# Kernel optimization log

Hardware: AMD Instinct MI355X
Metric: run time of the kernel (lower is better)

Reference implementation:

```python
import jax, jax.numpy as jnp
import numpy as np

D, H, L, V, BS = 1024, 16, 12, 50257, 2048
HD = D // H
EPS = 1e-5


def _ln(x, w, b):
    m = jnp.mean(x, -1, keepdims=True)
    v = jnp.mean(jnp.square(x - m), -1, keepdims=True)
    return (x - m) * jax.lax.rsqrt(v + EPS) * w + b


def setup_inputs() -> dict:
    key = jax.random.key(0)
    ks = jax.random.split(key, 10)
    B, T = 4, 1024
    s = 0.02
    return {
        "idx": jax.random.randint(ks[0], (B, T), 0, V),
        "targets": jax.random.randint(ks[1], (B, T), 0, V),
        "wte": s * jax.random.normal(ks[2], (V, D), jnp.float32),
        "wpe": s * jax.random.normal(ks[3], (BS, D), jnp.float32),
        "ln1_w": jnp.ones((L, D), jnp.float32),
        "ln1_b": jnp.zeros((L, D), jnp.float32),
        "qkv_w": s * jax.random.normal(ks[4], (L, D, 3 * D), jnp.float32),
        "qkv_b": jnp.zeros((L, 3 * D), jnp.float32),
        "o_w": s * jax.random.normal(ks[5], (L, D, D), jnp.float32),
        "o_b": jnp.zeros((L, D), jnp.float32),
        "ln2_w": jnp.ones((L, D), jnp.float32),
        "ln2_b": jnp.zeros((L, D), jnp.float32),
        "up_w": s * jax.random.normal(ks[6], (L, D, 4 * D), jnp.float32),
        "up_b": jnp.zeros((L, 4 * D), jnp.float32),
        "down_w": s * jax.random.normal(ks[7], (L, 4 * D, D), jnp.float32),
        "down_b": jnp.zeros((L, D), jnp.float32),
        "lnf_w": jnp.ones((D,), jnp.float32),
        "lnf_b": jnp.zeros((D,), jnp.float32),
        "lm_b": jnp.zeros((V,), jnp.float32),
    }


def _gpt(idx, targets, wte, wpe, ln1_w, ln1_b, qkv_w, qkv_b, o_w, o_b,
         ln2_w, ln2_b, up_w, up_b, down_w, down_b, lnf_w, lnf_b, lm_b):
    B, T = idx.shape
    x = wte[idx] + wpe[:T][None, :, :]  # [B,T,D]
    causal = jnp.tril(jnp.ones((T, T), bool))
    scale = HD ** -0.5

    def block(h, p):
        (l1w, l1b, qw, qb, ow, ob, l2w, l2b, uw, ub, dw, db) = p
        y = _ln(h, l1w, l1b)
        qkv = y @ qw + qb  # [B,T,3D]
        q, k, v = jnp.split(qkv, 3, axis=-1)
        q = q.reshape(B, T, H, HD)
        k = k.reshape(B, T, H, HD)
        v = v.reshape(B, T, H, HD)
        scores = jnp.einsum('bqhd,bkhd->bhqk', q, k) * scale
        scores = jnp.where(causal, scores, -jnp.inf)
        attn = jax.nn.softmax(scores, axis=-1)
        o = jnp.einsum('bhqk,bkhd->bqhd', attn, v).reshape(B, T, D)
        h = h + o @ ow + ob
        y = _ln(h, l2w, l2b)
        y = jax.nn.gelu(y @ uw + ub, approximate=False)
        h = h + y @ dw + db
        return h, None

    params = (ln1_w, ln1_b, qkv_w, qkv_b, o_w, o_b, ln2_w, ln2_b, up_w, up_b, down_w, down_b)
    x, _ = jax.lax.scan(block, x, params)
    x = _ln(x, lnf_w, lnf_b)
    logits = x @ wte.T + lm_b  # tied lm_head weight
    logp = jax.nn.log_softmax(logits, axis=-1)
    nll = -jnp.take_along_axis(logp, targets[..., None], axis=-1)[..., 0]
    loss = jnp.mean(nll)
    return logits, loss


def reference(idx, targets, wte, wpe, ln1_w, ln1_b, qkv_w, qkv_b, o_w, o_b,
              ln2_w, ln2_b, up_w, up_b, down_w, down_b, lnf_w, lnf_b, lm_b):
    return _gpt(idx, targets, wte, wpe, ln1_w, ln1_b, qkv_w, qkv_b, o_w, o_b,
                ln2_w, ln2_b, up_w, up_b, down_w, down_b, lnf_w, lnf_b, lm_b)
```

## Files before the change

### kernel.cpp

```cpp
#include <hip/hip_runtime.h>
#include <hip/hip_bf16.h>
#include <math.h>

typedef __attribute__((ext_vector_type(8))) short bfrag;
typedef __attribute__((ext_vector_type(4))) float f32x4;

static constexpr int Dm = 1024, Hh = 16, HD = 64, Ll = 12, Tt = 1024, Bb = 4;
static constexpr int Vv = 50257, Mrows = 4096;

__device__ inline unsigned short f2bf(float f) {
    unsigned u = __float_as_uint(f);
    u += 0x7fffu + ((u >> 16) & 1u);
    return (unsigned short)(u >> 16);
}
__device__ inline float bf2f(unsigned short s) {
    return __uint_as_float(((unsigned)s) << 16);
}

__device__ inline void gload16(const unsigned short* g, unsigned short* l) {
    __builtin_amdgcn_global_load_lds(
        (const __attribute__((address_space(1))) void*)g,
        (__attribute__((address_space(3))) void*)l, 16, 0, 0);
}

__global__ __launch_bounds__(256)
void embed_kernel(float* __restrict__ x, const float* __restrict__ wte,
                  const float* __restrict__ wpe, const int* __restrict__ idx) {
    int row = blockIdx.x;
    int t = row & (Tt - 1);
    int id = idx[row];
    int c = threadIdx.x * 4;
    float4 a = *reinterpret_cast<const float4*>(&wte[(size_t)id * Dm + c]);
    float4 p = *reinterpret_cast<const float4*>(&wpe[(size_t)t * Dm + c]);
    float4 o;
    o.x = a.x + p.x; o.y = a.y + p.y; o.z = a.z + p.z; o.w = a.w + p.w;
    *reinterpret_cast<float4*>(&x[(size_t)row * Dm + c]) = o;
}

__global__ __launch_bounds__(256)
void ln_kernel(unsigned short* __restrict__ y, const float* __restrict__ x,
               const float* __restrict__ w, const float* __restrict__ b) {
    int row = blockIdx.x;
    int tid = threadIdx.x;
    int lane = tid & 63, wv = tid >> 6;
    const float* xr = x + (size_t)row * Dm;
    float4 v = *reinterpret_cast<const float4*>(&xr[tid * 4]);
    float s1 = v.x + v.y + v.z + v.w;
    float s2 = v.x * v.x + v.y * v.y + v.z * v.z + v.w * v.w;
#pragma unroll
    for (int off = 1; off < 64; off <<= 1) {
        s1 += __shfl_xor(s1, off);
        s2 += __shfl_xor(s2, off);
    }
    __shared__ float r1[4], r2[4];
    if (lane == 0) { r1[wv] = s1; r2[wv] = s2; }
    __syncthreads();
    s1 = r1[0] + r1[1] + r1[2] + r1[3];
    s2 = r2[0] + r2[1] + r2[2] + r2[3];
    float mean = s1 * (1.0f / Dm);
    float var = s2 * (1.0f / Dm) - mean * mean;
    float rstd = rsqrtf(var + 1e-5f);
    float4 wvv = *reinterpret_cast<const float4*>(&w[tid * 4]);
    float4 bv = *reinterpret_cast<const float4*>(&b[tid * 4]);
    ushort4 o;
    o.x = f2bf((v.x - mean) * rstd * wvv.x + bv.x);
    o.y = f2bf((v.y - mean) * rstd * wvv.y + bv.y);
    o.z = f2bf((v.z - mean) * rstd * wvv.z + bv.z);
    o.w = f2bf((v.w - mean) * rstd * wvv.w + bv.w);
    *reinterpret_cast<ushort4*>(&y[(size_t)row * Dm + tid * 4]) = o;
}

__global__ __launch_bounds__(256)
void transpose_layer(const float* __restrict__ qw, const float* __restrict__ ow,
                     const float* __restrict__ uw, const float* __restrict__ dw,
                     unsigned short* __restrict__ wTq, unsigned short* __restrict__ wTo,
                     unsigned short* __restrict__ wTu, unsigned short* __restrict__ wTd) {
    __shared__ float t[32][33];
    int tb = blockIdx.x;
    const float* src; unsigned short* dst; int K, N, nx, base;
    if (tb < 3072)      { src = qw; dst = wTq; K = 1024; N = 3072; nx = 96;  base = 0; }
    else if (tb < 4096) { src = ow; dst = wTo; K = 1024; N = 1024; nx = 32;  base = 3072; }
    else if (tb < 8192) { src = uw; dst = wTu; K = 1024; N = 4096; nx = 128; base = 4096; }
    else                { src = dw; dst = wTd; K = 4096; N = 1024; nx = 32;  base = 8192; }
    int tt = tb - base;
    int n0 = (tt % nx) * 32, k0 = (tt / nx) * 32;
    int tid = threadIdx.x;
    int r = tid >> 3, c4 = (tid & 7) * 4;
    float4 v = *reinterpret_cast<const float4*>(&src[(size_t)(k0 + r) * N + n0 + c4]);
    t[r][c4] = v.x; t[r][c4 + 1] = v.y; t[r][c4 + 2] = v.z; t[r][c4 + 3] = v.w;
    __syncthreads();
    int nr = tid >> 3, kc = (tid & 7) * 4;
    ushort4 o;
    o.x = f2bf(t[kc][nr]);
    o.y = f2bf(t[kc + 1][nr]);
    o.z = f2bf(t[kc + 2][nr]);
    o.w = f2bf(t[kc + 3][nr]);
    *reinterpret_cast<ushort4*>(&dst[(size_t)(n0 + nr) * K + k0 + kc]) = o;
}

__global__ __launch_bounds__(128)
void cvt_rows(unsigned short* __restrict__ dst, const float* __restrict__ src) {
    int row = blockIdx.x;
    int t = threadIdx.x;
    const float* s = src + (size_t)row * Dm + t * 8;
    float4 f0 = *reinterpret_cast<const float4*>(s);
    float4 f1 = *reinterpret_cast<const float4*>(s + 4);
    ushort4 o0, o1;
    o0.x = f2bf(f0.x); o0.y = f2bf(f0.y); o0.z = f2bf(f0.z); o0.w = f2bf(f0.w);
    o1.x = f2bf(f1.x); o1.y = f2bf(f1.y); o1.z = f2bf(f1.z); o1.w = f2bf(f1.w);
    unsigned short* d = dst + (size_t)row * Dm + t * 8;
    *reinterpret_cast<ushort4*>(d) = o0;
    *reinterpret_cast<ushort4*>(d + 4) = o1;
}

template<int EPI, int GN>
__global__ __launch_bounds__(512, 1)
void gemm256(const unsigned short* __restrict__ A, const unsigned short* __restrict__ B,
             const float* __restrict__ bias, void* __restrict__ Cp,
             int Nv, int K, int ldc, int ncol) {
    __shared__ unsigned short As[4][256 * 32];
    __shared__ unsigned short Bs[4][256 * 32];
    const int tid = threadIdx.x;
    const int lane = tid & 63, w = tid >> 6;
    const int wr = w >> 2, wc = w & 3;
    const int g = lane >> 4, lr = lane & 15;
    const int slotk = (lr >> 1) & 3;

    const int gx = gridDim.x;
    int flat = blockIdx.y * gx + blockIdx.x;
    int nwg = gx * gridDim.y;
    {
        int q = nwg >> 3, rr = nwg & 7;
        int xcd = flat & 7, pos = flat >> 3;
        flat = ((xcd < rr) ? (xcd * (q + 1)) : (rr * (q + 1) + (xcd - rr) * q)) + pos;
    }
    const int bm = (flat % gx) * 256;
    const int bn = (flat / gx) * 256;

    const int srow = lane >> 2;
    const int gsrc = (lane & 3) ^ ((lane >> 3) & 3);
    const int rA0 = (w * 2 + 0) * 16 + srow;
    const int rA1 = (w * 2 + 1) * 16 + srow;
    const size_t aoff0 = (size_t)(bm + rA0) * K + gsrc * 8;
    const size_t aoff1 = (size_t)(bm + rA1) * K + gsrc * 8;
    int gb0 = bn + rA0, gb1 = bn + rA1;
    if (GN) { gb0 = (gb0 < Nv) ? gb0 : (Nv - 1); gb1 = (gb1 < Nv) ? gb1 : (Nv - 1); }
    const size_t boff0 = (size_t)gb0 * K + gsrc * 8;
    const size_t boff1 = (size_t)gb1 * K + gsrc * 8;
    unsigned short* lA0 = &As[0][(w * 2 + 0) * 512];
    unsigned short* lA1 = &As[0][(w * 2 + 1) * 512];
    unsigned short* lB0 = &Bs[0][(w * 2 + 0) * 512];
    unsigned short* lB1 = &Bs[0][(w * 2 + 1) * 512];

    const int nt = K >> 5;

    f32x4 acc[8][4];
#pragma unroll
    for (int i = 0; i < 8; ++i)
#pragma unroll
        for (int j = 0; j < 4; ++j)
#pragma unroll
            for (int r = 0; r < 4; ++r) acc[i][j][r] = 0.f;

#pragma unroll
    for (int tp = 0; tp < 3; ++tp) {
        const int kp = tp << 5;
        gload16(A + aoff0 + kp, lA0 + tp * 8192);
        gload16(B + boff0 + kp, lB0 + tp * 8192);
        gload16(A + aoff1 + kp, lA1 + tp * 8192);
        gload16(B + boff1 + kp, lB1 + tp * 8192);
    }
    asm volatile("s_waitcnt vmcnt(8)" ::: "memory");
    asm volatile("s_barrier" ::: "memory");

    for (int t = 0; t < nt; ++t) {
        const int bt = t & 3;
        const unsigned short* as = As[bt];
        const unsigned short* bs = Bs[bt];
        const int pf = t + 3;
        const int kp = pf << 5;
        const int so = (pf & 3) * 8192;

        bfrag bfr[4], af[4];
#pragma unroll
        for (int ni = 0; ni < 4; ++ni) {
            int row = wc * 64 + ni * 16 + lr;
            bfr[ni] = *reinterpret_cast<const bfrag*>(&bs[row * 32 + ((g ^ slotk) * 8)]);
        }
#pragma unroll
        for (int mi = 0; mi < 4; ++mi) {
            int row = wr * 128 + mi * 16 + lr;
            af[mi] = *reinterpret_cast<const bfrag*>(&as[row * 32 + ((g ^ slotk) * 8)]);
        }
        if (pf < nt) {
            gload16(A + aoff0 + kp, lA0 + so);
            gload16(B + boff0 + kp, lB0 + so);
        }
        asm volatile("s_barrier" ::: "memory");
        __builtin_amdgcn_s_setprio(1);
#pragma unroll
        for (int mi = 0; mi < 4; ++mi)
#pragma unroll
            for (int ni = 0; ni < 4; ++ni)
                acc[mi][ni] = __builtin_amdgcn_mfma_f32_16x16x32_bf16(
                    af[mi], bfr[ni], acc[mi][ni], 0, 0, 0);
        __builtin_amdgcn_s_setprio(0);
        asm volatile("s_barrier" ::: "memory");

#pragma unroll
        for (int mi = 0; mi < 4; ++mi) {
            int row = wr * 128 + (mi + 4) * 16 + lr;
            af[mi] = *reinterpret_cast<const bfrag*>(&as[row * 32 + ((g ^ slotk) * 8)]);
        }
        if (pf < nt) {
            gload16(A + aoff1 + kp, lA1 + so);
            gload16(B + boff1 + kp, lB1 + so);
        }
        asm volatile("s_barrier" ::: "memory");
        __builtin_amdgcn_s_setprio(1);
#pragma unroll
        for (int mi = 0; mi < 4; ++mi)
#pragma unroll
            for (int ni = 0; ni < 4; ++ni)
                acc[mi + 4][ni] = __builtin_amdgcn_mfma_f32_16x16x32_bf16(
                    af[mi], bfr[ni], acc[mi + 4][ni], 0, 0, 0);
        __builtin_amdgcn_s_setprio(0);
        if (t + 3 < nt)      asm volatile("s_waitcnt vmcnt(8)" ::: "memory");
        else if (t + 2 < nt) asm volatile("s_waitcnt vmcnt(4)" ::: "memory");
        else if (t + 1 < nt) asm volatile("s_waitcnt vmcnt(0)" ::: "memory");
        asm volatile("s_barrier" ::: "memory");
    }

    unsigned short* Cb = (unsigned short*)Cp;
    float* Cf = (float*)Cp;
#pragma unroll
    for (int ni = 0; ni < 4; ++ni) {
        int col = bn + wc * 64 + ni * 16 + lr;
        if (GN && col >= Nv) continue;
        int gcol = ncol + col;
        float bi = bias[gcol];
#pragma unroll
        for (int mi = 0; mi < 8; ++mi) {
            int row0 = bm + wr * 128 + mi * 16 + g * 4;
#pragma unroll
            for (int r = 0; r < 4; ++r) {
                int row = row0 + r;
                float v = acc[mi][ni][r] + bi;
                if (EPI == 0) {
                    Cb[(size_t)row * ldc + gcol] = f2bf(v);
                } else if (EPI == 1) {
                    v = 0.5f * v * (1.0f + erff(v * 0.70710678118654752f));
                    Cb[(size_t)row * ldc + gcol] = f2bf(v);
                } else {
                    Cf[(size_t)row * ldc + gcol] = v;
                }
            }
        }
    }
}

template<int EPI, int GN>
__global__ __launch_bounds__(256)
void gemm_mfma(const unsigned short* __restrict__ A, const unsigned short* __restrict__ B,
               const float* __restrict__ bias, const float* __restrict__ R,
               void* __restrict__ Cp, int M, int Nv, int K, int ldc, int ncol) {
    __shared__ unsigned short As[128 * 64];
    __shared__ unsigned short Bs[128 * 64];
    const int tid = threadIdx.x;
    const int lane = tid & 63, wid = tid >> 6;
    const int gx = gridDim.x;
    int flat = blockIdx.y * gx + blockIdx.x;
    int nwg = gx * gridDim.y;
    {
        int q = nwg >> 3, rr = nwg & 7;
        int xcd = flat & 7, pos = flat >> 3;
        flat = ((xcd < rr) ? (xcd * (q + 1)) : (rr * (q + 1) + (xcd - rr) * q)) + pos;
    }
    const int bm = (flat % gx) * 128;
    const int bn = (flat / gx) * 128;
    const int wr = wid >> 1, wc = wid & 1;
    const int g = lane >> 4, lr = lane & 15;
    const int l8 = lane >> 3;
    const int k8 = (lane & 7) ^ l8;

    f32x4 acc[4][4];
#pragma unroll
    for (int i = 0; i < 4; ++i)
#pragma unroll
        for (int j = 0; j < 4; ++j)
#pragma unroll
            for (int r = 0; r < 4; ++r) acc[i][j][r] = 0.f;

    for (int k0 = 0; k0 < K; k0 += 64) {
#pragma unroll
        for (int jj = 0; jj < 8; ++jj) {
            int j = wid * 8 + jj;
            if (j < 16) {
                int row = j * 8 + l8;
                gload16(&A[(size_t)(bm + row) * K + k0 + k8 * 8], &As[j * 512]);
            } else {
                int j16 = j - 16;
                int row = j16 * 8 + l8;
                int grow = bn + row;
                if (GN) grow = (grow < Nv) ? grow : (Nv - 1);
                gload16(&B[(size_t)grow * K + k0 + k8 * 8], &Bs[j16 * 512]);
            }
        }
        __syncthreads();
#pragma unroll
        for (int ks = 0; ks < 2; ++ks) {
            bfrag af[4], bfr[4];
#pragma unroll
            for (int i = 0; i < 4; ++i) {
                int ra = wr * 64 + i * 16 + lr;
                af[i] = *reinterpret_cast<const bfrag*>(
                    &As[ra * 64 + ((((ks << 2) | g) ^ (ra & 7)) * 8)]);
                int rb = wc * 64 + i * 16 + lr;
                bfr[i] = *reinterpret_cast<const bfrag*>(
                    &Bs[rb * 64 + ((((ks << 2) | g) ^ (rb & 7)) * 8)]);
            }
#pragma unroll
            for (int mi = 0; mi < 4; ++mi)
#pragma unroll
                for (int ni = 0; ni < 4; ++ni)
                    acc[mi][ni] = __builtin_amdgcn_mfma_f32_16x16x32_bf16(
                        af[mi], bfr[ni], acc[mi][ni], 0, 0, 0);
        }
        __syncthreads();
    }

    unsigned short* Cb = (unsigned short*)Cp;
    float* Cf = (float*)Cp;
#pragma unroll
    for (int ni = 0; ni < 4; ++ni) {
        int col = bn + wc * 64 + ni * 16 + lr;
        if (GN && col >= Nv) continue;
        int gcol = ncol + col;
        float bi = bias[gcol];
#pragma unroll
        for (int mi = 0; mi < 4; ++mi) {
            int row0 = bm + wr * 64 + mi * 16 + g * 4;
#pragma unroll
            for (int r = 0; r < 4; ++r) {
                int row = row0 + r;
                float v = acc[mi][ni][r] + bi;
                if (EPI == 0) {
                    Cb[(size_t)row * ldc + gcol] = f2bf(v);
                } else if (EPI == 1) {
                    v = 0.5f * v * (1.0f + erff(v * 0.70710678118654752f));
                    Cb[(size_t)row * ldc + gcol] = f2bf(v);
                } else if (EPI == 2) {
                    Cf[(size_t)row * ldc + gcol] = R[(size_t)row * ldc + gcol] + v;
                } else {
                    Cf[(size_t)row * ldc + gcol] = v;
                }
            }
        }
    }
}

__global__ __launch_bounds__(256)
void attn_mfma(const unsigned short* __restrict__ qkv, unsigned short* __restrict__ ob) {
    const int bq = blockIdx.x;
    const int h = blockIdx.y;
    const int b = blockIdx.z;
    const int tid = threadIdx.x, lane = tid & 63, w = tid >> 6;
    const int g = lane >> 4, lr = lane & 15;
    const int qg0 = bq * 128 + w * 32;

    __shared__ unsigned short Kt[64 * 72];
    __shared__ unsigned short Vt[64 * 72];
    __shared__ unsigned short Pl[4][32 * 72];
    unsigned short* Plw = Pl[w];

    bfrag aq[2][2];
#pragma unroll
    for (int qs = 0; qs < 2; ++qs)
#pragma unroll
        for (int ks = 0; ks < 2; ++ks) {
            int row = qg0 + qs * 16 + lr;
            aq[qs][ks] = *reinterpret_cast<const bfrag*>(
                &qkv[(size_t)(b * Tt + row) * 3072 + h * 64 + ks * 32 + g * 8]);
        }

    float mrow[2][4], lrow[2][4], osc[2][4];
    f32x4 oacc[2][4];
#pragma unroll
    for (int qs = 0; qs < 2; ++qs)
#pragma unroll
        for (int r = 0; r < 4; ++r) { mrow[qs][r] = -3.0e38f; lrow[qs][r] = 0.f; }
#pragma unroll
    for (int qs = 0; qs < 2; ++qs)
#pragma unroll
        for (int dn = 0; dn < 4; ++dn)
#pragma unroll
            for (int r = 0; r < 4; ++r) oacc[qs][dn][r] = 0.f;

    const int ntile = 2 * bq + 2;
    for (int kt = 0; kt < ntile; ++kt) {
        {
            int row = tid >> 2, seg = tid & 3;
            const unsigned short* sk =
                &qkv[(size_t)(b * Tt + kt * 64 + row) * 3072 + Dm + h * 64 + seg * 16];
            bfrag kv0 = *(const bfrag*)sk;
            bfrag kv1 = *(const bfrag*)(sk + 8);
            *reinterpret_cast<bfrag*>(&Kt[row * 72 + seg * 16]) = kv0;
            *reinterpret_cast<bfrag*>(&Kt[row * 72 + seg * 16 + 8]) = kv1;
            const uint4* sv = reinterpret_cast<const uint4*>(
                &qkv[(size_t)(b * Tt + kt * 64 + row) * 3072 + 2 * Dm + h * 64 + seg * 16]);
            uint4 u0 = sv[0], u1 = sv[1];
            uint4 a, r0, r1;
            a.x = (seg & 1) ? u0.y : u0.x; a.y = (seg & 1) ? u0.z : u0.y;
            a.z = (seg & 1) ? u0.w : u0.z; a.w = (seg & 1) ? u0.x : u0.w;
            r0.x = (seg & 2) ? a.z : a.x; r0.y = (seg & 2) ? a.w : a.y;
            r0.z = (seg & 2) ? a.x : a.z; r0.w = (seg & 2) ? a.y : a.w;
            a.x = (seg & 1) ? u1.y : u1.x; a.y = (seg & 1) ? u1.z : u1.y;
            a.z = (seg & 1) ? u1.w : u1.z; a.w = (seg & 1) ? u1.x : u1.w;
            r1.x = (seg & 2) ? a.z : a.x; r1.y = (seg & 2) ? a.w : a.y;
            r1.z = (seg & 2) ? a.x : a.z; r1.w = (seg & 2) ? a.y : a.w;
            unsigned w0[4] = {r0.x, r0.y, r0.z, r0.w};
            unsigned w1[4] = {r1.x, r1.y, r1.z, r1.w};
#pragma unroll
            for (int i = 0; i < 8; ++i) {
                int j = (i + 2 * seg) & 7;
                unsigned ww = w0[i >> 1];
                unsigned short val = (i & 1) ? (unsigned short)(ww >> 16)
                                             : (unsigned short)(ww & 0xffff);
                Vt[(seg * 16 + j) * 72 + row] = val;
            }
#pragma unroll
            for (int i = 0; i < 8; ++i) {
                int j = (i + 2 * seg) & 7;
                unsigned ww = w1[i >> 1];
                unsigned short val = (i & 1) ? (unsigned short)(ww >> 16)
                                             : (unsigned short)(ww & 0xffff);
                Vt[(seg * 16 + 8 + j) * 72 + row] = val;
            }
        }
        __syncthreads();

        bool active = (kt * 64 <= qg0 + 31);
        if (active) {
            f32x4 s[2][4];
#pragma unroll
            for (int qs = 0; qs < 2; ++qs)
#pragma unroll
                for (int n = 0; n < 4; ++n)
#pragma unroll
                    for (int r = 0; r < 4; ++r) s[qs][n][r] = 0.f;
            bfrag bk[4][2];
#pragma unroll
            for (int n = 0; n < 4; ++n)
#pragma unroll
                for (int ks = 0; ks < 2; ++ks)
                    bk[n][ks] = *reinterpret_cast<const bfrag*>(
                        &Kt[(n * 16 + lr) * 72 + ks * 32 + g * 8]);
#pragma unroll
            for (int qs = 0; qs < 2; ++qs)
#pragma unroll
                for (int n = 0; n < 4; ++n)
#pragma unroll
                    for (int ks = 0; ks < 2; ++ks)
                        s[qs][n] = __builtin_amdgcn_mfma_f32_16x16x32_bf16(
                            aq[qs][ks], bk[n][ks], s[qs][n], 0, 0, 0);

            bool mayMask = (kt * 64 + 63 > qg0);
            float pv[2][4][4];
#pragma unroll
            for (int qs = 0; qs < 2; ++qs) {
#pragma unroll
                for (int r = 0; r < 4; ++r) {
                    int qrow = qg0 + qs * 16 + g * 4 + r;
                    float v[4];
#pragma unroll
                    for (int n = 0; n < 4; ++n) {
                        float sv = s[qs][n][r] * 0.125f;
                        if (mayMask && (kt * 64 + n * 16 + lr > qrow)) sv = -3.0e38f;
                        v[n] = sv;
                    }
                    float tmax = fmaxf(fmaxf(v[0], v[1]), fmaxf(v[2], v[3]));
                    tmax = fmaxf(tmax, __shfl_xor(tmax, 1));
                    tmax = fmaxf(tmax, __shfl_xor(tmax, 2));
                    tmax = fmaxf(tmax, __shfl_xor(tmax, 4));
                    tmax = fmaxf(tmax, __shfl_xor(tmax, 8));
                    float mold = mrow[qs][r];
                    float mnew = fmaxf(mold, tmax);
                    float scl = expf(mold - mnew);
                    float psum = 0.f;
#pragma unroll
                    for (int n = 0; n < 4; ++n) {
                        float p = expf(v[n] - mnew);
                        pv[qs][n][r] = p;
                        psum += p;
                    }
                    psum += __shfl_xor(psum, 1);
                    psum += __shfl_xor(psum, 2);
                    psum += __shfl_xor(psum, 4);
                    psum += __shfl_xor(psum, 8);
                    lrow[qs][r] = lrow[qs][r] * scl + psum;
                    mrow[qs][r] = mnew;
                    osc[qs][r] = scl;
                }
            }
#pragma unroll
            for (int qs = 0; qs < 2; ++qs)
#pragma unroll
                for (int dn = 0; dn < 4; ++dn)
#pragma unroll
                    for (int r = 0; r < 4; ++r) oacc[qs][dn][r] *= osc[qs][r];
#pragma unroll
            for (int qs = 0; qs < 2; ++qs)
#pragma unroll
                for (int n = 0; n < 4; ++n)
#pragma unroll
                    for (int r = 0; r < 4; ++r)
                        Plw[(qs * 16 + g * 4 + r) * 72 + n * 16 + lr] = f2bf(pv[qs][n][r]);
            asm volatile("s_waitcnt lgkmcnt(0)" ::: "memory");
            bfrag ap[2][2], bv[4][2];
#pragma unroll
            for (int qs = 0; qs < 2; ++qs)
#pragma unroll
                for (int ks = 0; ks < 2; ++ks)
                    ap[qs][ks] = *reinterpret_cast<const bfrag*>(
                        &Plw[(qs * 16 + lr) * 72 + ks * 32 + g * 8]);
#pragma unroll
            for (int dn = 0; dn < 4; ++dn)
#pragma unroll
                for (int ks = 0; ks < 2; ++ks)
                    bv[dn][ks] = *reinterpret_cast<const bfrag*>(
                        &Vt[(dn * 16 + lr) * 72 + ks * 32 + g * 8]);
#pragma unroll
            for (int qs = 0; qs < 2; ++qs)
#pragma unroll
                for (int dn = 0; dn < 4; ++dn)
#pragma unroll
                    for (int ks = 0; ks < 2; ++ks)
                        oacc[qs][dn] = __builtin_amdgcn_mfma_f32_16x16x32_bf16(
                            ap[qs][ks], bv[dn][ks], oacc[qs][dn], 0, 0, 0);
        }
        __syncthreads();
    }

#pragma unroll
    for (int qs = 0; qs < 2; ++qs)
#pragma unroll
        for (int r = 0; r < 4; ++r) {
            float rinv = 1.0f / lrow[qs][r];
            int qrow = qg0 + qs * 16 + g * 4 + r;
#pragma unroll
            for (int dn = 0; dn < 4; ++dn)
                ob[(size_t)(b * Tt + qrow) * Dm + h * 64 + dn * 16 + lr] =
                    f2bf(oacc[qs][dn][r] * rinv);
        }
}

__global__ __launch_bounds__(512)
void loss_row_kernel(float* __restrict__ nll, const float* __restrict__ logits,
                     const int* __restrict__ targets) {
    const int row = blockIdx.x;
    const int tid = threadIdx.x;
    const int lane = tid & 63, wv = tid >> 6;
    const float* lr = logits + (size_t)row * Vv;

    const int lead = (4 - (row & 3)) & 3;
    const int nvec = (Vv - lead) >> 2;
    const int tail = Vv - lead - (nvec << 2);

    float m = -3.0e38f, s = 0.f;
    if (tid < lead) {
        float v = lr[tid];
        m = v; s = 1.f;
    }
    for (int k = tid; k < nvec; k += 512) {
        float4 v = *reinterpret_cast<const float4*>(lr + lead + (k << 2));
        float tm = fmaxf(fmaxf(v.x, v.y), fmaxf(v.z, v.w));
        float nm = fmaxf(m, tm);
        s = s * __expf(m - nm)
          + __expf(v.x - nm) + __expf(v.y - nm) + __expf(v.z - nm) + __expf(v.w - nm);
        m = nm;
    }
    if (tid < tail) {
        float v = lr[lead + (nvec << 2) + tid];
        float nm = fmaxf(m, v);
        s = s * __expf(m - nm) + __expf(v - nm);
        m = nm;
    }
#pragma unroll
    for (int off = 1; off < 64; off <<= 1) {
        float om = __shfl_xor(m, off);
        float os = __shfl_xor(s, off);
        float nm = fmaxf(m, om);
        s = s * __expf(m - nm) + os * __expf(om - nm);
        m = nm;
    }
    __shared__ float rm[8], rs[8];
    if (lane == 0) { rm[wv] = m; rs[wv] = s; }
    __syncthreads();
    if (tid == 0) {
        float M = rm[0];
#pragma unroll
        for (int i = 1; i < 8; ++i) M = fmaxf(M, rm[i]);
        float S = 0.f;
#pragma unroll
        for (int i = 0; i < 8; ++i) S += rs[i] * __expf(rm[i] - M);
        float lse = M + __logf(S);
        nll[row] = lse - lr[targets[row]];
    }
}

__global__ __launch_bounds__(256)
void loss_reduce_kernel(float* __restrict__ loss, const float* __restrict__ nll) {
    int tid = threadIdx.x;
    __shared__ float red[256];
    float s = 0.f;
    for (int j = tid; j < Mrows; j += 256) s += nll[j];
    red[tid] = s;
    __syncthreads();
    for (int st = 128; st > 0; st >>= 1) {
        if (tid < st) red[tid] += red[tid + st];
        __syncthreads();
    }
    if (tid == 0) *loss = red[0] * (1.0f / Mrows);
}

extern "C" void kernel_launch(void* const* d_in, const int* in_sizes, int n_in,
                              void* d_out, int out_size, void* d_ws, size_t ws_size,
                              hipStream_t stream) {
    const int* idx = (const int*)d_in[0];
    const int* targets = (const int*)d_in[1];
    const float* wte = (const float*)d_in[2];
    const float* wpe = (const float*)d_in[3];
    const float* ln1_w = (const float*)d_in[4];
    const float* ln1_b = (const float*)d_in[5];
    const float* qkv_w = (const float*)d_in[6];
    const float* qkv_b = (const float*)d_in[7];
    const float* o_w = (const float*)d_in[8];
    const float* o_b = (const float*)d_in[9];
    const float* ln2_w = (const float*)d_in[10];
    const float* ln2_b = (const float*)d_in[11];
    const float* up_w = (const float*)d_in[12];
    const float* up_b = (const float*)d_in[13];
    const float* down_w = (const float*)d_in[14];
    const float* down_b = (const float*)d_in[15];
    const float* lnf_w = (const float*)d_in[16];
    const float* lnf_b = (const float*)d_in[17];
    const float* lm_b = (const float*)d_in[18];

    float* logits = (float*)d_out;
    char* ws = (char*)d_ws;
    const size_t MB = 1 << 20;
    float* x            = (float*)(ws);
    unsigned short* y   = (unsigned short*)(ws + 16 * MB);
    unsigned short* qkv = (unsigned short*)(ws + 24 * MB);
    unsigned short* ob  = (unsigned short*)(ws + 48 * MB);
    unsigned short* up  = (unsigned short*)(ws + 56 * MB);
    unsigned short* wTq = (unsigned short*)(ws + 88 * MB);
    unsigned short* wTo = (unsigned short*)(ws + 96 * MB);
    unsigned short* wTu = (unsigned short*)(ws + 100 * MB);
    unsigned short* wTd = (unsigned short*)(ws + 112 * MB);
    float* nll          = (float*)(ws + 127 * MB);
    unsigned short* wbf = (unsigned short*)(ws + 24 * MB);

    embed_kernel<<<Mrows, 256, 0, stream>>>(x, wte, wpe, idx);

    for (int l = 0; l < Ll; ++l) {
        ln_kernel<<<Mrows, 256, 0, stream>>>(y, x, ln1_w + l * Dm, ln1_b + l * Dm);
        transpose_layer<<<12288, 256, 0, stream>>>(
            qkv_w + (size_t)l * Dm * 3 * Dm, o_w + (size_t)l * Dm * Dm,
            up_w + (size_t)l * Dm * 4 * Dm, down_w + (size_t)l * 4 * Dm * Dm,
            wTq, wTo, wTu, wTd);
        gemm256<0, 0><<<dim3(Mrows / 256, 3 * Dm / 256), 512, 0, stream>>>(
            y, wTq, qkv_b + (size_t)l * 3 * Dm, qkv, 3 * Dm, Dm, 3 * Dm, 0);
        attn_mfma<<<dim3(8, Hh, Bb), 256, 0, stream>>>(qkv, ob);
        gemm_mfma<2, 0><<<dim3(Mrows / 128, Dm / 128), 256, 0, stream>>>(
            ob, wTo, o_b + (size_t)l * Dm, x, x, Mrows, Dm, Dm, Dm, 0);
        ln_kernel<<<Mrows, 256, 0, stream>>>(y, x, ln2_w + l * Dm, ln2_b + l * Dm);
        gemm256<1, 0><<<dim3(Mrows / 256, 4 * Dm / 256), 512, 0, stream>>>(
            y, wTu, up_b + (size_t)l * 4 * Dm, up, 4 * Dm, Dm, 4 * Dm, 0);
        gemm_mfma<2, 0><<<dim3(Mrows / 128, Dm / 128), 256, 0, stream>>>(
            up, wTd, down_b + (size_t)l * Dm, x, x, Mrows, Dm, 4 * Dm, Dm, 0);
    }

    ln_kernel<<<Mrows, 256, 0, stream>>>(y, x, lnf_w, lnf_b);

    cvt_rows<<<Vv, 128, 0, stream>>>(wbf, wte);
    gemm256<3, 1><<<dim3(Mrows / 256, (Vv + 255) / 256), 512, 0, stream>>>(
        y, wbf, lm_b, logits, Vv, Dm, Vv, 0);

    loss_row_kernel<<<Mrows, 512, 0, stream>>>(nll, logits, targets);
    loss_reduce_kernel<<<1, 256, 0, stream>>>(logits + (size_t)Mrows * Vv, nll);
}
```

Measured before the change: 4.881 ms.

## Pipeline 128x128 GEMMs with 4-stage async LDS prefetch and merge gemm256 halves

Replaces the simple single-buffered gemm_mfma with gemm128p, a 4-stage global_load_lds pipeline using 32-wide K slices, XOR swizzle and vmcnt-based waits. QKV, out-proj and down-proj now use it. gemm256 loads all 8 A fragments at once, drops the mid-iteration barriers and issues all prefetches together, and its launch bound is raised to allow 2 blocks per CU. The aim is to hide global load latency and reduce barrier stalls, at the cost of more registers, which may cause spills under the tighter bound. Moving QKV to 128 tiles also launches more, smaller blocks.

Result: faster. 4.622 ms (-5.3%).

```diff
diff --git a/kernel.cpp b/kernel.cpp
--- a/kernel.cpp
+++ b/kernel.cpp
@@ -114,7 +114,7 @@
 }
 
 template<int EPI, int GN>
-__global__ __launch_bounds__(512, 1)
+__global__ __launch_bounds__(512, 2)
 void gemm256(const unsigned short* __restrict__ A, const unsigned short* __restrict__ B,
              const float* __restrict__ bias, void* __restrict__ Cp,
              int Nv, int K, int ldc, int ncol) {
@@ -181,49 +181,30 @@
         const int kp = pf << 5;
         const int so = (pf & 3) * 8192;
 
-        bfrag bfr[4], af[4];
+        bfrag bfr[4], af[8];
 #pragma unroll
         for (int ni = 0; ni < 4; ++ni) {
             int row = wc * 64 + ni * 16 + lr;
             bfr[ni] = *reinterpret_cast<const bfrag*>(&bs[row * 32 + ((g ^ slotk) * 8)]);
         }
 #pragma unroll
-        for (int mi = 0; mi < 4; ++mi) {
+        for (int mi = 0; mi < 8; ++mi) {
             int row = wr * 128 + mi * 16 + lr;
             af[mi] = *reinterpret_cast<const bfrag*>(&as[row * 32 + ((g ^ slotk) * 8)]);
         }
         if (pf < nt) {
             gload16(A + aoff0 + kp, lA0 + so);
             gload16(B + boff0 + kp, lB0 + so);
-        }
-        asm volatile("s_barrier" ::: "memory");
+            gload16(A + aoff1 + kp, lA1 + so);
+            gload16(B + boff1 + kp, lB1 + so);
+        }
         __builtin_amdgcn_s_setprio(1);
 #pragma unroll
-        for (int mi = 0; mi < 4; ++mi)
+        for (int mi = 0; mi < 8; ++mi)
 #pragma unroll
             for (int ni = 0; ni < 4; ++ni)
                 acc[mi][ni] = __builtin_amdgcn_mfma_f32_16x16x32_bf16(
                     af[mi], bfr[ni], acc[mi][ni], 0, 0, 0);
-        __builtin_amdgcn_s_setprio(0);
-        asm volatile("s_barrier" ::: "memory");
-
-#pragma unroll
-        for (int mi = 0; mi < 4; ++mi) {
-            int row = wr * 128 + (mi + 4) * 16 + lr;
-            af[mi] = *reinterpret_cast<const bfrag*>(&as[row * 32 + ((g ^ slotk) * 8)]);
-        }
-        if (pf < nt) {
-            gload16(A + aoff1 + kp, lA1 + so);
-            gload16(B + boff1 + kp, lB1 + so);
-        }
-        asm volatile("s_barrier" ::: "memory");
-        __builtin_amdgcn_s_setprio(1);
-#pragma unroll
-        for (int mi = 0; mi < 4; ++mi)
-#pragma unroll
-            for (int ni = 0; ni < 4; ++ni)
-                acc[mi + 4][ni] = __builtin_amdgcn_mfma_f32_16x16x32_bf16(
-                    af[mi], bfr[ni], acc[mi + 4][ni], 0, 0, 0);
         __builtin_amdgcn_s_setprio(0);
         if (t + 3 < nt)      asm volatile("s_waitcnt vmcnt(8)" ::: "memory");
         else if (t + 2 < nt) asm volatile("s_waitcnt vmcnt(4)" ::: "memory");
@@ -259,15 +240,19 @@
     }
 }
 
-template<int EPI, int GN>
-__global__ __launch_bounds__(256)
-void gemm_mfma(const unsigned short* __restrict__ A, const unsigned short* __restrict__ B,
-               const float* __restrict__ bias, const float* __restrict__ R,
-               void* __restrict__ Cp, int M, int Nv, int K, int ldc, int ncol) {
-    __shared__ unsigned short As[128 * 64];
-    __shared__ unsigned short Bs[128 * 64];
+template<int EPI>
+__global__ __launch_bounds__(256, 2)
+void gemm128p(const unsigned short* __restrict__ A, const unsigned short* __restrict__ B,
+              const float* __restrict__ bias, const float* __restrict__ R,
+              void* __restrict__ Cp, int K, int ldc) {
+    __shared__ unsigned short As[4][128 * 32];
+    __shared__ unsigned short Bs[4][128 * 32];
     const int tid = threadIdx.x;
-    const int lane = tid & 63, wid = tid >> 6;
+    const int lane = tid & 63, w = tid >> 6;
+    const int wr = w >> 1, wc = w & 1;
+    const int g = lane >> 4, lr = lane & 15;
+    const int slotk = (lr >> 1) & 3;
+
     const int gx = gridDim.x;
     int flat = blockIdx.y * gx + blockIdx.x;
     int nwg = gx * gridDim.y;
@@ -278,10 +263,21 @@
     }
     const int bm = (flat % gx) * 128;
     const int bn = (flat / gx) * 128;
-    const int wr = wid >> 1, wc = wid & 1;
-    const int g = lane >> 4, lr = lane & 15;
-    const int l8 = lane >> 3;
-    const int k8 = (lane & 7) ^ l8;
+
+    const int srow = lane >> 2;
+    const int gsrc = (lane & 3) ^ ((lane >> 3) & 3);
+    const int rA0 = (w * 2 + 0) * 16 + srow;
+    const int rA1 = (w * 2 + 1) * 16 + srow;
+    const size_t aoff0 = (size_t)(bm + rA0) * K + gsrc * 8;
+    const size_t aoff1 = (size_t)(bm + rA1) * K + gsrc * 8;
+    const size_t boff0 = (size_t)(bn + rA0) * K + gsrc * 8;
+    const size_t boff1 = (size_t)(bn + rA1) * K + gsrc * 8;
+    unsigned short* lA0 = &As[0][(w * 2 + 0) * 512];
+    unsigned short* lA1 = &As[0][(w * 2 + 1) * 512];
+    unsigned short* lB0 = &Bs[0][(w * 2 + 0) * 512];
+    unsigned short* lB1 = &Bs[0][(w * 2 + 1) * 512];
+
+    const int nt = K >> 5;
 
     f32x4 acc[4][4];
 #pragma unroll
@@ -291,42 +287,51 @@
 #pragma unroll
             for (int r = 0; r < 4; ++r) acc[i][j][r] = 0.f;
 
-    for (int k0 = 0; k0 < K; k0 += 64) {
-#pragma unroll
-        for (int jj = 0; jj < 8; ++jj) {
-            int j = wid * 8 + jj;
-            if (j < 16) {
-                int row = j * 8 + l8;
-                gload16(&A[(size_t)(bm + row) * K + k0 + k8 * 8], &As[j * 512]);
-            } else {
-                int j16 = j - 16;
-                int row = j16 * 8 + l8;
-                int grow = bn + row;
-                if (GN) grow = (grow < Nv) ? grow : (Nv - 1);
-                gload16(&B[(size_t)grow * K + k0 + k8 * 8], &Bs[j16 * 512]);
-            }
-        }
-        __syncthreads();
-#pragma unroll
-        for (int ks = 0; ks < 2; ++ks) {
-            bfrag af[4], bfr[4];
-#pragma unroll
-            for (int i = 0; i < 4; ++i) {
-                int ra = wr * 64 + i * 16 + lr;
-                af[i] = *reinterpret_cast<const bfrag*>(
-                    &As[ra * 64 + ((((ks << 2) | g) ^ (ra & 7)) * 8)]);
-                int rb = wc * 64 + i * 16 + lr;
-                bfr[i] = *reinterpret_cast<const bfrag*>(
-                    &Bs[rb * 64 + ((((ks << 2) | g) ^ (rb & 7)) * 8)]);
-            }
-#pragma unroll
-            for (int mi = 0; mi < 4; ++mi)
-#pragma unroll
-                for (int ni = 0; ni < 4; ++ni)
-                    acc[mi][ni] = __builtin_amdgcn_mfma_f32_16x16x32_bf16(
-                        af[mi], bfr[ni], acc[mi][ni], 0, 0, 0);
-        }
-        __syncthreads();
+#pragma unroll
+    for (int tp = 0; tp < 3; ++tp) {
+        const int kp = tp << 5;
+        gload16(A + aoff0 + kp, lA0 + tp * 4096);
+        gload16(B + boff0 + kp, lB0 + tp * 4096);
+        gload16(A + aoff1 + kp, lA1 + tp * 4096);
+        gload16(B + boff1 + kp, lB1 + tp * 4096);
+    }
+    asm volatile("s_waitcnt vmcnt(8)" ::: "memory");
+    asm volatile("s_barrier" ::: "memory");
+
+    for (int t = 0; t < nt; ++t) {
+        const int bt = t & 3;
+        const unsigned short* as = As[bt];
+        const unsigned short* bs = Bs[bt];
+        const int pf = t + 3;
+        const int kp = pf << 5;
+        const int so = (pf & 3) * 4096;
+
+        bfrag af[4], bfr[4];
+#pragma unroll
+        for (int i = 0; i < 4; ++i) {
+            int ra = wr * 64 + i * 16 + lr;
+            af[i] = *reinterpret_cast<const bfrag*>(&as[ra * 32 + ((g ^ slotk) * 8)]);
+            int rb = wc * 64 + i * 16 + lr;
+            bfr[i] = *reinterpret_cast<const bfrag*>(&bs[rb * 32 + ((g ^ slotk) * 8)]);
+        }
+        if (pf < nt) {
+            gload16(A + aoff0 + kp, lA0 + so);
+            gload16(B + boff0 + kp, lB0 + so);
+            gload16(A + aoff1 + kp, lA1 + so);
+            gload16(B + boff1 + kp, lB1 + so);
+        }
+        __builtin_amdgcn_s_setprio(1);
+#pragma unroll
+        for (int mi = 0; mi < 4; ++mi)
+#pragma unroll
+            for (int ni = 0; ni < 4; ++ni)
+                acc[mi][ni] = __builtin_amdgcn_mfma_f32_16x16x32_bf16(
+                    af[mi], bfr[ni], acc[mi][ni], 0, 0, 0);
+        __builtin_amdgcn_s_setprio(0);
+        if (t + 3 < nt)      asm volatile("s_waitcnt vmcnt(8)" ::: "memory");
+        else if (t + 2 < nt) asm volatile("s_waitcnt vmcnt(4)" ::: "memory");
+        else if (t + 1 < nt) asm volatile("s_waitcnt vmcnt(0)" ::: "memory");
+        asm volatile("s_barrier" ::: "memory");
     }
 
     unsigned short* Cb = (unsigned short*)Cp;
@@ -334,9 +339,7 @@
 #pragma unroll
     for (int ni = 0; ni < 4; ++ni) {
         int col = bn + wc * 64 + ni * 16 + lr;
-        if (GN && col >= Nv) continue;
-        int gcol = ncol + col;
-        float bi = bias[gcol];
+        float bi = bias[col];
 #pragma unroll
         for (int mi = 0; mi < 4; ++mi) {
             int row0 = bm + wr * 64 + mi * 16 + g * 4;
@@ -345,14 +348,9 @@
                 int row = row0 + r;
                 float v = acc[mi][ni][r] + bi;
                 if (EPI == 0) {
-                    Cb[(size_t)row * ldc + gcol] = f2bf(v);
-                } else if (EPI == 1) {
-                    v = 0.5f * v * (1.0f + erff(v * 0.70710678118654752f));
-                    Cb[(size_t)row * ldc + gcol] = f2bf(v);
-                } else if (EPI == 2) {
-                    Cf[(size_t)row * ldc + gcol] = R[(size_t)row * ldc + gcol] + v;
+                    Cb[(size_t)row * ldc + col] = f2bf(v);
                 } else {
-                    Cf[(size_t)row * ldc + gcol] = v;
+                    Cf[(size_t)row * ldc + col] = R[(size_t)row * ldc + col] + v;
                 }
             }
         }
@@ -669,16 +667,16 @@
             qkv_w + (size_t)l * Dm * 3 * Dm, o_w + (size_t)l * Dm * Dm,
             up_w + (size_t)l * Dm * 4 * Dm, down_w + (size_t)l * 4 * Dm * Dm,
             wTq, wTo, wTu, wTd);
-        gemm256<0, 0><<<dim3(Mrows / 256, 3 * Dm / 256), 512, 0, stream>>>(
-            y, wTq, qkv_b + (size_t)l * 3 * Dm, qkv, 3 * Dm, Dm, 3 * Dm, 0);
+        gemm128p<0><<<dim3(Mrows / 128, 3 * Dm / 128), 256, 0, stream>>>(
+            y, wTq, qkv_b + (size_t)l * 3 * Dm, nullptr, qkv, Dm, 3 * Dm);
         attn_mfma<<<dim3(8, Hh, Bb), 256, 0, stream>>>(qkv, ob);
-        gemm_mfma<2, 0><<<dim3(Mrows / 128, Dm / 128), 256, 0, stream>>>(
-            ob, wTo, o_b + (size_t)l * Dm, x, x, Mrows, Dm, Dm, Dm, 0);
+        gemm128p<2><<<dim3(Mrows / 128, Dm / 128), 256, 0, stream>>>(
+            ob, wTo, o_b + (size_t)l * Dm, x, x, Dm, Dm);
         ln_kernel<<<Mrows, 256, 0, stream>>>(y, x, ln2_w + l * Dm, ln2_b + l * Dm);
         gemm256<1, 0><<<dim3(Mrows / 256, 4 * Dm / 256), 512, 0, stream>>>(
             y, wTu, up_b + (size_t)l * 4 * Dm, up, 4 * Dm, Dm, 4 * Dm, 0);
-        gemm_mfma<2, 0><<<dim3(Mrows / 128, Dm / 128), 256, 0, stream>>>(
-            up, wTd, down_b + (size_t)l * Dm, x, x, Mrows, Dm, 4 * Dm, Dm, 0);
+        gemm128p<2><<<dim3(Mrows / 128, Dm / 128), 256, 0, stream>>>(
+            up, wTd, down_b + (size_t)l * Dm, x, x, 4 * Dm, Dm);
     }
 
     ln_kernel<<<Mrows, 256, 0, stream>>>(y, x, lnf_w, lnf_b);
```
